# Performance work log

Measured on AMD Instinct MI355X. Metric: run time of the kernel, lower is better.

The kernel has to match this reference:

```python
import jax, jax.numpy as jnp
import numpy as np

E, T, D, N_RBF, N_SBF = 262144, 1048576, 128, 6, 42


def setup_inputs() -> dict:
    key = jax.random.key(0)
    ks = jax.random.split(key, 24)
    s = 0.05
    inp = {
        "m_ji": jax.random.normal(ks[0], (E, D), jnp.float32),
        "e_rbf": jax.random.normal(ks[1], (E, N_RBF), jnp.float32),
        "a_sbf": jax.random.normal(ks[2], (T, N_SBF), jnp.float32),
        "nbr_list": jax.random.randint(ks[3], (E, 2), 0, 65536),
        "kj_idx": jax.random.randint(ks[4], (T,), 0, E),
        "ji_idx": jax.random.randint(ks[5], (T,), 0, E),
        # edge branch params
        "We": jax.random.normal(ks[6], (N_RBF, D), jnp.float32) * s,
        "W_e1": jax.random.normal(ks[7], (D, D), jnp.float32) * s,
        "b_e1": jnp.zeros((D,), jnp.float32),
        "W_e2": jax.random.normal(ks[8], (D, D), jnp.float32) * s,
        "b_e2": jnp.zeros((D,), jnp.float32),
        "W_e3": jax.random.normal(ks[9], (D, D), jnp.float32) * s,
        "b_e3": jnp.zeros((D,), jnp.float32),
        "W_e4": jax.random.normal(ks[10], (D, D), jnp.float32) * s,
        # angle branch params
        "Wa": jax.random.normal(ks[11], (N_SBF, D), jnp.float32) * s,
        "W_a1": jax.random.normal(ks[12], (D, D), jnp.float32) * s,
        "b_a1": jnp.zeros((D,), jnp.float32),
        "W_a2": jax.random.normal(ks[13], (D, D), jnp.float32) * s,
        "b_a2": jnp.zeros((D,), jnp.float32),
        "W_a3": jax.random.normal(ks[14], (D, D), jnp.float32) * s,
        "b_a3": jnp.zeros((D,), jnp.float32),
        "W_a4": jax.random.normal(ks[15], (D, D), jnp.float32) * s,
    }
    return inp


def _mlp(x, W1, b1, W2, b2, W3, b3, W4):
    x = jax.nn.silu(x @ W1 + b1)
    x = jax.nn.silu(x @ W2 + b2)
    x = jax.nn.silu(x @ W3 + b3)
    return x @ W4


def reference(m_ji, e_rbf, a_sbf, nbr_list, kj_idx, ji_idx,
              We, W_e1, b_e1, W_e2, b_e2, W_e3, b_e3, W_e4,
              Wa, W_a1, b_a1, W_a2, b_a2, W_a3, b_a3, W_a4):
    # edge branch: project rbf to embed dim, gate by edge messages  [E, D]
    edge_feats = _mlp((e_rbf @ We) * m_ji, W_e1, b_e1, W_e2, b_e2, W_e3, b_e3, W_e4)
    # angle branch: project sbf, gate by triplet-gathered message sum  [T, D]
    angle_gate = m_ji[kj_idx] + m_ji[ji_idx]
    angle_feats = _mlp((a_sbf @ Wa) * angle_gate, W_a1, b_a1, W_a2, b_a2, W_a3, b_a3, W_a4)
    return (edge_feats, angle_feats)
```

## Files before the change

kernel.cpp:

```cpp
#include <hip/hip_runtime.h>
#include <stdint.h>

typedef __attribute__((ext_vector_type(8))) short bf16x8;
typedef __attribute__((ext_vector_type(4))) float f32x4;
typedef __attribute__((ext_vector_type(8))) unsigned short us8;

#define T_CNT 1048576
#define E_CNT 262144

static __device__ __forceinline__ unsigned short f2bf_u(float f) {
  __bf16 h = (__bf16)f;
  return __builtin_bit_cast(unsigned short, h);
}
static __device__ __forceinline__ uint32_t pack2bf(float a, float b) {
  return (uint32_t)f2bf_u(a) | ((uint32_t)f2bf_u(b) << 16);
}
static __device__ __forceinline__ float silu_f(float v) {
  float e = __builtin_amdgcn_exp2f(v * -1.44269504088896341f);
  return v * __builtin_amdgcn_rcpf(1.0f + e);
}
static __device__ __forceinline__ bf16x8 frag8(f32x4 a, f32x4 b) {
  bf16x8 r;
  r[0] = (short)f2bf_u(a[0]); r[1] = (short)f2bf_u(a[1]);
  r[2] = (short)f2bf_u(a[2]); r[3] = (short)f2bf_u(a[3]);
  r[4] = (short)f2bf_u(b[0]); r[5] = (short)f2bf_u(b[1]);
  r[6] = (short)f2bf_u(b[2]); r[7] = (short)f2bf_u(b[3]);
  return r;
}

__global__ __launch_bounds__(256)
__attribute__((amdgpu_waves_per_eu(4, 5)))
void angle_kernel(
    const float* __restrict__ m_ji, const float* __restrict__ a_sbf,
    const int* __restrict__ kj, const int* __restrict__ ji,
    const float* __restrict__ b1, const float* __restrict__ b2,
    const float* __restrict__ b3,
    const char* __restrict__ wt4, const char* __restrict__ waT,
    float* __restrict__ out)
{
  __shared__ __align__(16) char xbA[16384];
  __shared__ __align__(16) char xbB[16384];
  const int tid = threadIdx.x, lane = tid & 63, w = tid >> 6;
  const int l15 = lane & 15, q = lane >> 4;
  const int rs = (l15 & 7) << 4;
  const size_t tb = (size_t)blockIdx.x * 64;
  const int cb = w * 32;

  bf16x8 wa[2][2];
  #pragma unroll
  for (int ct = 0; ct < 2; ++ct)
    #pragma unroll
    for (int ks = 0; ks < 2; ++ks)
      wa[ct][ks] = *(const bf16x8*)(waT + (((w * 2 + ct) * 2 + ks) << 10) + lane * 16);

  int ikj[4], iji[4];
  #pragma unroll
  for (int g = 0; g < 4; ++g) {
    ikj[g] = kj[tb + g * 16 + l15];
    iji[g] = ji[tb + g * 16 + l15];
  }

  f32x4 pk[2][2], pj[2][2];
  auto gissue = [&](int g) {
    const float* bk = m_ji + (size_t)ikj[g] * 128 + cb + q * 4;
    const float* bj = m_ji + (size_t)iji[g] * 128 + cb + q * 4;
    pk[g & 1][0] = *(const f32x4*)(bk);
    pk[g & 1][1] = *(const f32x4*)(bk + 16);
    pj[g & 1][0] = *(const f32x4*)(bj);
    pj[g & 1][1] = *(const f32x4*)(bj + 16);
  };
  gissue(0); gissue(1);

  #pragma unroll
  for (int rg = 0; rg < 4; ++rg) {
    const int row = rg * 16 + l15;
    const float* ap = a_sbf + (tb + row) * 42;
    f32x4 a0 = *(const f32x4*)(ap + q * 8);
    f32x4 a1 = *(const f32x4*)(ap + q * 8 + 4);
    f32x4 c0 = {0.f, 0.f, 0.f, 0.f}, c1 = {0.f, 0.f, 0.f, 0.f};
    if (q == 0) { c0 = *(const f32x4*)(ap + 32); c1 = *(const f32x4*)(ap + 36); }
    else if (q == 1) { float2 t = *(const float2*)(ap + 40); c0[0] = t.x; c0[1] = t.y; }
    bf16x8 f0 = frag8(a0, a1);
    bf16x8 f1 = frag8(c0, c1);
    f32x4 acc0 = {0.f, 0.f, 0.f, 0.f}, acc1 = {0.f, 0.f, 0.f, 0.f};
    acc0 = __builtin_amdgcn_mfma_f32_16x16x32_bf16(wa[0][0], f0, acc0, 0, 0, 0);
    acc0 = __builtin_amdgcn_mfma_f32_16x16x32_bf16(wa[0][1], f1, acc0, 0, 0, 0);
    acc1 = __builtin_amdgcn_mfma_f32_16x16x32_bf16(wa[1][0], f0, acc1, 0, 0, 0);
    acc1 = __builtin_amdgcn_mfma_f32_16x16x32_bf16(wa[1][1], f1, acc1, 0, 0, 0);
    f32x4 g0 = pk[rg & 1][0] + pj[rg & 1][0];
    f32x4 g1 = pk[rg & 1][1] + pj[rg & 1][1];
    if (rg < 2) gissue(rg + 2);
    uint2 u0, u1;
    u0.x = pack2bf(acc0[0] * g0[0], acc0[1] * g0[1]);
    u0.y = pack2bf(acc0[2] * g0[2], acc0[3] * g0[3]);
    u1.x = pack2bf(acc1[0] * g1[0], acc1[1] * g1[1]);
    u1.y = pack2bf(acc1[2] * g1[2], acc1[3] * g1[3]);
    *(uint2*)(xbA + ((row * 256 + w * 64 + q * 8) ^ rs)) = u0;
    *(uint2*)(xbA + ((row * 256 + w * 64 + 32 + q * 8) ^ rs)) = u1;
  }
  __syncthreads();

  #pragma unroll
  for (int L = 0; L < 4; ++L) {
    const char* src = (L & 1) ? xbB : xbA;
    char* dst = (L & 1) ? xbA : xbB;
    bf16x8 wf[2][4];
    #pragma unroll
    for (int ct = 0; ct < 2; ++ct)
      #pragma unroll
      for (int ks = 0; ks < 4; ++ks)
        wf[ct][ks] = *(const bf16x8*)(wt4 + (L << 15) + (((w * 2 + ct) * 4 + ks) << 10) + lane * 16);
    if (L < 3) {
      const float* bp = (L == 0) ? b1 : (L == 1) ? b2 : b3;
      f32x4 bv0 = *(const f32x4*)(bp + cb + q * 4);
      f32x4 bv1 = *(const f32x4*)(bp + cb + 16 + q * 4);
      #pragma unroll
      for (int rg = 0; rg < 4; ++rg) {
        const int row = rg * 16 + l15;
        f32x4 acc0 = {0.f, 0.f, 0.f, 0.f}, acc1 = {0.f, 0.f, 0.f, 0.f};
        #pragma unroll
        for (int ks = 0; ks < 4; ++ks) {
          bf16x8 xf = *(const bf16x8*)(src + ((row * 256 + ks * 64 + q * 16) ^ rs));
          acc0 = __builtin_amdgcn_mfma_f32_16x16x32_bf16(wf[0][ks], xf, acc0, 0, 0, 0);
          acc1 = __builtin_amdgcn_mfma_f32_16x16x32_bf16(wf[1][ks], xf, acc1, 0, 0, 0);
        }
        uint2 u0, u1;
        u0.x = pack2bf(silu_f(acc0[0] + bv0[0]), silu_f(acc0[1] + bv0[1]));
        u0.y = pack2bf(silu_f(acc0[2] + bv0[2]), silu_f(acc0[3] + bv0[3]));
        u1.x = pack2bf(silu_f(acc1[0] + bv1[0]), silu_f(acc1[1] + bv1[1]));
        u1.y = pack2bf(silu_f(acc1[2] + bv1[2]), silu_f(acc1[3] + bv1[3]));
        *(uint2*)(dst + ((row * 256 + w * 64 + q * 8) ^ rs)) = u0;
        *(uint2*)(dst + ((row * 256 + w * 64 + 32 + q * 8) ^ rs)) = u1;
      }
      __syncthreads();
    } else {
      #pragma unroll
      for (int rg = 0; rg < 4; ++rg) {
        const int row = rg * 16 + l15;
        f32x4 acc0 = {0.f, 0.f, 0.f, 0.f}, acc1 = {0.f, 0.f, 0.f, 0.f};
        #pragma unroll
        for (int ks = 0; ks < 4; ++ks) {
          bf16x8 xf = *(const bf16x8*)(src + ((row * 256 + ks * 64 + q * 16) ^ rs));
          acc0 = __builtin_amdgcn_mfma_f32_16x16x32_bf16(wf[0][ks], xf, acc0, 0, 0, 0);
          acc1 = __builtin_amdgcn_mfma_f32_16x16x32_bf16(wf[1][ks], xf, acc1, 0, 0, 0);
        }
        float* op = out + (tb + row) * 128 + cb + q * 4;
        __builtin_nontemporal_store(acc0, (f32x4*)(op));
        __builtin_nontemporal_store(acc1, (f32x4*)(op + 16));
      }
    }
  }
}

__global__ __launch_bounds__(256)
__attribute__((amdgpu_waves_per_eu(4, 5)))
void edge_kernel(
    const float* __restrict__ m_ji, const float* __restrict__ e_rbf,
    const float* __restrict__ b1, const float* __restrict__ b2,
    const float* __restrict__ b3,
    const char* __restrict__ wt4, const char* __restrict__ weT,
    float* __restrict__ out)
{
  __shared__ __align__(16) char xbA[16384];
  __shared__ __align__(16) char xbB[16384];
  const int tid = threadIdx.x, lane = tid & 63, w = tid >> 6;
  const int l15 = lane & 15, q = lane >> 4;
  const int rs = (l15 & 7) << 4;
  const size_t tb = (size_t)blockIdx.x * 64;
  const int cb = w * 32;

  bf16x8 we[2];
  #pragma unroll
  for (int ct = 0; ct < 2; ++ct)
    we[ct] = *(const bf16x8*)(weT + ((w * 2 + ct) << 10) + lane * 16);

  f32x4 mr[2][2];
  auto missue = [&](int g) {
    const float* bm = m_ji + (tb + g * 16 + l15) * 128 + cb + q * 4;
    mr[g & 1][0] = *(const f32x4*)(bm);
    mr[g & 1][1] = *(const f32x4*)(bm + 16);
  };
  missue(0); missue(1);

  #pragma unroll
  for (int rg = 0; rg < 4; ++rg) {
    const int row = rg * 16 + l15;
    const float* ep = e_rbf + (tb + row) * 6;
    f32x4 a0 = {0.f, 0.f, 0.f, 0.f}, a1 = {0.f, 0.f, 0.f, 0.f};
    if (q == 0) {
      a0 = *(const f32x4*)(ep);
      float2 t = *(const float2*)(ep + 4);
      a1[0] = t.x; a1[1] = t.y;
    }
    bf16x8 ef = frag8(a0, a1);
    f32x4 acc0 = {0.f, 0.f, 0.f, 0.f}, acc1 = {0.f, 0.f, 0.f, 0.f};
    acc0 = __builtin_amdgcn_mfma_f32_16x16x32_bf16(we[0], ef, acc0, 0, 0, 0);
    acc1 = __builtin_amdgcn_mfma_f32_16x16x32_bf16(we[1], ef, acc1, 0, 0, 0);
    f32x4 g0 = mr[rg & 1][0];
    f32x4 g1 = mr[rg & 1][1];
    if (rg < 2) missue(rg + 2);
    uint2 u0, u1;
    u0.x = pack2bf(acc0[0] * g0[0], acc0[1] * g0[1]);
    u0.y = pack2bf(acc0[2] * g0[2], acc0[3] * g0[3]);
    u1.x = pack2bf(acc1[0] * g1[0], acc1[1] * g1[1]);
    u1.y = pack2bf(acc1[2] * g1[2], acc1[3] * g1[3]);
    *(uint2*)(xbA + ((row * 256 + w * 64 + q * 8) ^ rs)) = u0;
    *(uint2*)(xbA + ((row * 256 + w * 64 + 32 + q * 8) ^ rs)) = u1;
  }
  __syncthreads();

  #pragma unroll
  for (int L = 0; L < 4; ++L) {
    const char* src = (L & 1) ? xbB : xbA;
    char* dst = (L & 1) ? xbA : xbB;
    bf16x8 wf[2][4];
    #pragma unroll
    for (int ct = 0; ct < 2; ++ct)
      #pragma unroll
      for (int ks = 0; ks < 4; ++ks)
        wf[ct][ks] = *(const bf16x8*)(wt4 + (L << 15) + (((w * 2 + ct) * 4 + ks) << 10) + lane * 16);
    if (L < 3) {
      const float* bp = (L == 0) ? b1 : (L == 1) ? b2 : b3;
      f32x4 bv0 = *(const f32x4*)(bp + cb + q * 4);
      f32x4 bv1 = *(const f32x4*)(bp + cb + 16 + q * 4);
      #pragma unroll
      for (int rg = 0; rg < 4; ++rg) {
        const int row = rg * 16 + l15;
        f32x4 acc0 = {0.f, 0.f, 0.f, 0.f}, acc1 = {0.f, 0.f, 0.f, 0.f};
        #pragma unroll
        for (int ks = 0; ks < 4; ++ks) {
          bf16x8 xf = *(const bf16x8*)(src + ((row * 256 + ks * 64 + q * 16) ^ rs));
          acc0 = __builtin_amdgcn_mfma_f32_16x16x32_bf16(wf[0][ks], xf, acc0, 0, 0, 0);
          acc1 = __builtin_amdgcn_mfma_f32_16x16x32_bf16(wf[1][ks], xf, acc1, 0, 0, 0);
        }
        uint2 u0, u1;
        u0.x = pack2bf(silu_f(acc0[0] + bv0[0]), silu_f(acc0[1] + bv0[1]));
        u0.y = pack2bf(silu_f(acc0[2] + bv0[2]), silu_f(acc0[3] + bv0[3]));
        u1.x = pack2bf(silu_f(acc1[0] + bv1[0]), silu_f(acc1[1] + bv1[1]));
        u1.y = pack2bf(silu_f(acc1[2] + bv1[2]), silu_f(acc1[3] + bv1[3]));
        *(uint2*)(dst + ((row * 256 + w * 64 + q * 8) ^ rs)) = u0;
        *(uint2*)(dst + ((row * 256 + w * 64 + 32 + q * 8) ^ rs)) = u1;
      }
      __syncthreads();
    } else {
      #pragma unroll
      for (int rg = 0; rg < 4; ++rg) {
        const int row = rg * 16 + l15;
        f32x4 acc0 = {0.f, 0.f, 0.f, 0.f}, acc1 = {0.f, 0.f, 0.f, 0.f};
        #pragma unroll
        for (int ks = 0; ks < 4; ++ks) {
          bf16x8 xf = *(const bf16x8*)(src + ((row * 256 + ks * 64 + q * 16) ^ rs));
          acc0 = __builtin_amdgcn_mfma_f32_16x16x32_bf16(wf[0][ks], xf, acc0, 0, 0, 0);
          acc1 = __builtin_amdgcn_mfma_f32_16x16x32_bf16(wf[1][ks], xf, acc1, 0, 0, 0);
        }
        float* op = out + (tb + row) * 128 + cb + q * 4;
        __builtin_nontemporal_store(acc0, (f32x4*)(op));
        __builtin_nontemporal_store(acc1, (f32x4*)(op + 16));
      }
    }
  }
}

__global__ void prep_kernel(
    const float* __restrict__ W0, const float* __restrict__ W1,
    const float* __restrict__ W2, const float* __restrict__ W3,
    const float* __restrict__ W4, const float* __restrict__ W5,
    const float* __restrict__ W6, const float* __restrict__ W7,
    const float* __restrict__ Wa, const float* __restrict__ We,
    char* __restrict__ ws)
{
  const int gid = blockIdx.x * 256 + threadIdx.x;
  const int lane = gid & 63;
  const int l15 = lane & 15, q = lane >> 4;
  if (gid < 16384) {
    const int mat = gid >> 11;
    const int ctks = (gid & 2047) >> 6;
    const int n = (ctks >> 2) * 16 + l15;
    const int k0 = (ctks & 3) * 32 + q * 8;
    const float* W;
    switch (mat) {
      case 0: W = W0; break; case 1: W = W1; break;
      case 2: W = W2; break; case 3: W = W3; break;
      case 4: W = W4; break; case 5: W = W5; break;
      case 6: W = W6; break; default: W = W7; break;
    }
    us8 v;
    #pragma unroll
    for (int j = 0; j < 8; ++j) v[j] = f2bf_u(W[(size_t)(k0 + j) * 128 + n]);
    *(us8*)(ws + mat * 32768 + ctks * 1024 + lane * 16) = v;
  } else if (gid < 17408) {
    const int g = gid - 16384;
    const int ctks = g >> 6;
    const int n = (ctks >> 1) * 16 + l15;
    const int k0 = (ctks & 1) * 32 + q * 8;
    us8 v;
    #pragma unroll
    for (int j = 0; j < 8; ++j) {
      const int k = k0 + j;
      v[j] = (k < 42) ? f2bf_u(Wa[(size_t)k * 128 + n]) : (unsigned short)0;
    }
    *(us8*)(ws + 262144 + ctks * 1024 + lane * 16) = v;
  } else if (gid < 17920) {
    const int g = gid - 17408;
    const int ct = g >> 6;
    const int n = ct * 16 + l15;
    const int k0 = q * 8;
    us8 v;
    #pragma unroll
    for (int j = 0; j < 8; ++j) {
      const int k = k0 + j;
      v[j] = (k < 6) ? f2bf_u(We[(size_t)k * 128 + n]) : (unsigned short)0;
    }
    *(us8*)(ws + 278528 + ct * 1024 + lane * 16) = v;
  }
}

extern "C" void kernel_launch(void* const* d_in, const int* in_sizes, int n_in,
                              void* d_out, int out_size, void* d_ws, size_t ws_size,
                              hipStream_t stream) {
  (void)in_sizes; (void)n_in; (void)out_size; (void)ws_size;
  const float* m_ji  = (const float*)d_in[0];
  const float* e_rbf = (const float*)d_in[1];
  const float* a_sbf = (const float*)d_in[2];
  const int*   kj    = (const int*)d_in[4];
  const int*   ji    = (const int*)d_in[5];
  const float* We    = (const float*)d_in[6];
  const float* We1   = (const float*)d_in[7];
  const float* be1   = (const float*)d_in[8];
  const float* We2   = (const float*)d_in[9];
  const float* be2   = (const float*)d_in[10];
  const float* We3   = (const float*)d_in[11];
  const float* be3   = (const float*)d_in[12];
  const float* We4   = (const float*)d_in[13];
  const float* Wa    = (const float*)d_in[14];
  const float* Wa1   = (const float*)d_in[15];
  const float* ba1   = (const float*)d_in[16];
  const float* Wa2   = (const float*)d_in[17];
  const float* ba2   = (const float*)d_in[18];
  const float* Wa3   = (const float*)d_in[19];
  const float* ba3   = (const float*)d_in[20];
  const float* Wa4   = (const float*)d_in[21];
  char* ws = (char*)d_ws;
  float* out = (float*)d_out;

  prep_kernel<<<70, 256, 0, stream>>>(
      We1, We2, We3, We4, Wa1, Wa2, Wa3, Wa4, Wa, We, ws);
  edge_kernel<<<E_CNT / 64, 256, 0, stream>>>(
      m_ji, e_rbf, be1, be2, be3, ws, ws + 278528, out);
  angle_kernel<<<T_CNT / 64, 256, 0, stream>>>(
      m_ji, a_sbf, kj, ji, ba1, ba2, ba3, ws + 131072, ws + 262144,
      out + (size_t)E_CNT * 128);
}
```

Baseline: 525.6 us.

## Split angle branch into gather/projection kernel and MLP kernel via workspace

Splits the angle branch in two when the workspace is large enough. The first kernel does the gather of m_ji rows, the sbf projection and the gating, and writes a bf16 activation buffer to the workspace. The second kernel streams that buffer into LDS with global_load_lds and runs the 4-layer MLP. The goal is to keep the latency-bound random gathers out of the MFMA-heavy kernel and let each kernel use the occupancy that suits it. The cost is an extra round trip of about 256 MB of intermediate data through global memory, and the waves_per_eu hints are dropped.

```diff
diff --git a/kernel.cpp b/kernel.cpp
--- a/kernel.cpp
+++ b/kernel.cpp
@@ -4,6 +4,8 @@
 typedef __attribute__((ext_vector_type(8))) short bf16x8;
 typedef __attribute__((ext_vector_type(4))) float f32x4;
 typedef __attribute__((ext_vector_type(8))) unsigned short us8;
+typedef __attribute__((ext_vector_type(2))) unsigned int u32x2;
+typedef __bf16 bf16v2 __attribute__((ext_vector_type(2)));
 
 #define T_CNT 1048576
 #define E_CNT 262144
@@ -13,93 +15,33 @@
   return __builtin_bit_cast(unsigned short, h);
 }
 static __device__ __forceinline__ uint32_t pack2bf(float a, float b) {
-  return (uint32_t)f2bf_u(a) | ((uint32_t)f2bf_u(b) << 16);
+  bf16v2 t; t[0] = (__bf16)a; t[1] = (__bf16)b;
+  return __builtin_bit_cast(uint32_t, t);
 }
 static __device__ __forceinline__ float silu_f(float v) {
   float e = __builtin_amdgcn_exp2f(v * -1.44269504088896341f);
   return v * __builtin_amdgcn_rcpf(1.0f + e);
 }
 static __device__ __forceinline__ bf16x8 frag8(f32x4 a, f32x4 b) {
-  bf16x8 r;
-  r[0] = (short)f2bf_u(a[0]); r[1] = (short)f2bf_u(a[1]);
-  r[2] = (short)f2bf_u(a[2]); r[3] = (short)f2bf_u(a[3]);
-  r[4] = (short)f2bf_u(b[0]); r[5] = (short)f2bf_u(b[1]);
-  r[6] = (short)f2bf_u(b[2]); r[7] = (short)f2bf_u(b[3]);
-  return r;
-}
-
-__global__ __launch_bounds__(256)
-__attribute__((amdgpu_waves_per_eu(4, 5)))
-void angle_kernel(
-    const float* __restrict__ m_ji, const float* __restrict__ a_sbf,
-    const int* __restrict__ kj, const int* __restrict__ ji,
+  union { bf16x8 v; uint32_t u[4]; } r;
+  r.u[0] = pack2bf(a[0], a[1]); r.u[1] = pack2bf(a[2], a[3]);
+  r.u[2] = pack2bf(b[0], b[1]); r.u[3] = pack2bf(b[2], b[3]);
+  return r.v;
+}
+static __device__ __forceinline__ void gl_lds16(const void* g, void* l) {
+  __builtin_amdgcn_global_load_lds(
+      (const __attribute__((address_space(1))) void*)g,
+      (__attribute__((address_space(3))) void*)l, 16, 0, 0);
+}
+
+static __device__ __forceinline__ void mlp4(
+    char* __restrict__ xbA, char* __restrict__ xbB,
+    const char* __restrict__ wt4,
     const float* __restrict__ b1, const float* __restrict__ b2,
-    const float* __restrict__ b3,
-    const char* __restrict__ wt4, const char* __restrict__ waT,
-    float* __restrict__ out)
-{
-  __shared__ __align__(16) char xbA[16384];
-  __shared__ __align__(16) char xbB[16384];
-  const int tid = threadIdx.x, lane = tid & 63, w = tid >> 6;
-  const int l15 = lane & 15, q = lane >> 4;
-  const int rs = (l15 & 7) << 4;
-  const size_t tb = (size_t)blockIdx.x * 64;
+    const float* __restrict__ b3, float* __restrict__ outT,
+    int l15, int q, int w, int rs)
+{
   const int cb = w * 32;
-
-  bf16x8 wa[2][2];
-  #pragma unroll
-  for (int ct = 0; ct < 2; ++ct)
-    #pragma unroll
-    for (int ks = 0; ks < 2; ++ks)
-      wa[ct][ks] = *(const bf16x8*)(waT + (((w * 2 + ct) * 2 + ks) << 10) + lane * 16);
-
-  int ikj[4], iji[4];
-  #pragma unroll
-  for (int g = 0; g < 4; ++g) {
-    ikj[g] = kj[tb + g * 16 + l15];
-    iji[g] = ji[tb + g * 16 + l15];
-  }
-
-  f32x4 pk[2][2], pj[2][2];
-  auto gissue = [&](int g) {
-    const float* bk = m_ji + (size_t)ikj[g] * 128 + cb + q * 4;
-    const float* bj = m_ji + (size_t)iji[g] * 128 + cb + q * 4;
-    pk[g & 1][0] = *(const f32x4*)(bk);
-    pk[g & 1][1] = *(const f32x4*)(bk + 16);
-    pj[g & 1][0] = *(const f32x4*)(bj);
-    pj[g & 1][1] = *(const f32x4*)(bj + 16);
-  };
-  gissue(0); gissue(1);
-
-  #pragma unroll
-  for (int rg = 0; rg < 4; ++rg) {
-    const int row = rg * 16 + l15;
-    const float* ap = a_sbf + (tb + row) * 42;
-    f32x4 a0 = *(const f32x4*)(ap + q * 8);
-    f32x4 a1 = *(const f32x4*)(ap + q * 8 + 4);
-    f32x4 c0 = {0.f, 0.f, 0.f, 0.f}, c1 = {0.f, 0.f, 0.f, 0.f};
-    if (q == 0) { c0 = *(const f32x4*)(ap + 32); c1 = *(const f32x4*)(ap + 36); }
-    else if (q == 1) { float2 t = *(const float2*)(ap + 40); c0[0] = t.x; c0[1] = t.y; }
-    bf16x8 f0 = frag8(a0, a1);
-    bf16x8 f1 = frag8(c0, c1);
-    f32x4 acc0 = {0.f, 0.f, 0.f, 0.f}, acc1 = {0.f, 0.f, 0.f, 0.f};
-    acc0 = __builtin_amdgcn_mfma_f32_16x16x32_bf16(wa[0][0], f0, acc0, 0, 0, 0);
-    acc0 = __builtin_amdgcn_mfma_f32_16x16x32_bf16(wa[0][1], f1, acc0, 0, 0, 0);
-    acc1 = __builtin_amdgcn_mfma_f32_16x16x32_bf16(wa[1][0], f0, acc1, 0, 0, 0);
-    acc1 = __builtin_amdgcn_mfma_f32_16x16x32_bf16(wa[1][1], f1, acc1, 0, 0, 0);
-    f32x4 g0 = pk[rg & 1][0] + pj[rg & 1][0];
-    f32x4 g1 = pk[rg & 1][1] + pj[rg & 1][1];
-    if (rg < 2) gissue(rg + 2);
-    uint2 u0, u1;
-    u0.x = pack2bf(acc0[0] * g0[0], acc0[1] * g0[1]);
-    u0.y = pack2bf(acc0[2] * g0[2], acc0[3] * g0[3]);
-    u1.x = pack2bf(acc1[0] * g1[0], acc1[1] * g1[1]);
-    u1.y = pack2bf(acc1[2] * g1[2], acc1[3] * g1[3]);
-    *(uint2*)(xbA + ((row * 256 + w * 64 + q * 8) ^ rs)) = u0;
-    *(uint2*)(xbA + ((row * 256 + w * 64 + 32 + q * 8) ^ rs)) = u1;
-  }
-  __syncthreads();
-
   #pragma unroll
   for (int L = 0; L < 4; ++L) {
     const char* src = (L & 1) ? xbB : xbA;
@@ -109,7 +51,7 @@
     for (int ct = 0; ct < 2; ++ct)
       #pragma unroll
       for (int ks = 0; ks < 4; ++ks)
-        wf[ct][ks] = *(const bf16x8*)(wt4 + (L << 15) + (((w * 2 + ct) * 4 + ks) << 10) + lane * 16);
+        wf[ct][ks] = *(const bf16x8*)(wt4 + (L << 15) + (((w * 2 + ct) * 4 + ks) << 10) + (l15 | (q << 4)) * 16);
     if (L < 3) {
       const float* bp = (L == 0) ? b1 : (L == 1) ? b2 : b3;
       f32x4 bv0 = *(const f32x4*)(bp + cb + q * 4);
@@ -117,7 +59,7 @@
       #pragma unroll
       for (int rg = 0; rg < 4; ++rg) {
         const int row = rg * 16 + l15;
-        f32x4 acc0 = {0.f, 0.f, 0.f, 0.f}, acc1 = {0.f, 0.f, 0.f, 0.f};
+        f32x4 acc0 = {0.f,0.f,0.f,0.f}, acc1 = {0.f,0.f,0.f,0.f};
         #pragma unroll
         for (int ks = 0; ks < 4; ++ks) {
           bf16x8 xf = *(const bf16x8*)(src + ((row * 256 + ks * 64 + q * 16) ^ rs));
@@ -137,14 +79,14 @@
       #pragma unroll
       for (int rg = 0; rg < 4; ++rg) {
         const int row = rg * 16 + l15;
-        f32x4 acc0 = {0.f, 0.f, 0.f, 0.f}, acc1 = {0.f, 0.f, 0.f, 0.f};
+        f32x4 acc0 = {0.f,0.f,0.f,0.f}, acc1 = {0.f,0.f,0.f,0.f};
         #pragma unroll
         for (int ks = 0; ks < 4; ++ks) {
           bf16x8 xf = *(const bf16x8*)(src + ((row * 256 + ks * 64 + q * 16) ^ rs));
           acc0 = __builtin_amdgcn_mfma_f32_16x16x32_bf16(wf[0][ks], xf, acc0, 0, 0, 0);
           acc1 = __builtin_amdgcn_mfma_f32_16x16x32_bf16(wf[1][ks], xf, acc1, 0, 0, 0);
         }
-        float* op = out + (tb + row) * 128 + cb + q * 4;
+        float* op = outT + (size_t)row * 128 + cb + q * 4;
         __builtin_nontemporal_store(acc0, (f32x4*)(op));
         __builtin_nontemporal_store(acc1, (f32x4*)(op + 16));
       }
@@ -152,13 +94,85 @@
   }
 }
 
-__global__ __launch_bounds__(256)
-__attribute__((amdgpu_waves_per_eu(4, 5)))
-void edge_kernel(
-    const float* __restrict__ m_ji, const float* __restrict__ e_rbf,
+__global__ __launch_bounds__(256) void angle_proj_kernel(
+    const float* __restrict__ m_ji, const float* __restrict__ a_sbf,
+    const int* __restrict__ kj, const int* __restrict__ ji,
+    const char* __restrict__ waT, char* __restrict__ x0)
+{
+  const int tid = threadIdx.x, lane = tid & 63, w = tid >> 6;
+  const int l15 = lane & 15, q = lane >> 4;
+  const int rs = (l15 & 7) << 4;
+  const size_t tb = (size_t)blockIdx.x * 64;
+  const int rl = w * 16 + l15;
+  const size_t grow = tb + rl;
+
+  const int ikj = kj[grow], iji = ji[grow];
+  const float* bk = m_ji + (size_t)ikj * 128 + q * 4;
+  const float* bj = m_ji + (size_t)iji * 128 + q * 4;
+
+  f32x4 pk[4], pj[4];
+  #pragma unroll
+  for (int g = 0; g < 4; ++g) {
+    pk[g] = *(const f32x4*)(bk + g * 16);
+    pj[g] = *(const f32x4*)(bj + g * 16);
+  }
+
+  const float* ap = a_sbf + grow * 42;
+  f32x4 a0 = *(const f32x4*)(ap + q * 8);
+  f32x4 a1 = *(const f32x4*)(ap + q * 8 + 4);
+  f32x4 c0 = {0.f,0.f,0.f,0.f}, c1 = {0.f,0.f,0.f,0.f};
+  if (q == 0) { c0 = *(const f32x4*)(ap + 32); c1 = *(const f32x4*)(ap + 36); }
+  else if (q == 1) { float2 t = *(const float2*)(ap + 40); c0[0] = t.x; c0[1] = t.y; }
+  bf16x8 f0 = frag8(a0, a1);
+  bf16x8 f1 = frag8(c0, c1);
+
+  char* xrow = x0 + tb * 256 + rl * 256;
+  #pragma unroll
+  for (int c = 0; c < 8; ++c) {
+    bf16x8 wa0 = *(const bf16x8*)(waT + ((c * 2 + 0) << 10) + lane * 16);
+    bf16x8 wa1 = *(const bf16x8*)(waT + ((c * 2 + 1) << 10) + lane * 16);
+    f32x4 acc = {0.f,0.f,0.f,0.f};
+    acc = __builtin_amdgcn_mfma_f32_16x16x32_bf16(wa0, f0, acc, 0, 0, 0);
+    acc = __builtin_amdgcn_mfma_f32_16x16x32_bf16(wa1, f1, acc, 0, 0, 0);
+    f32x4 g = pk[c & 3] + pj[c & 3];
+    if (c < 4) {
+      pk[c & 3] = *(const f32x4*)(bk + (c + 4) * 16);
+      pj[c & 3] = *(const f32x4*)(bj + (c + 4) * 16);
+    }
+    u32x2 u;
+    u[0] = pack2bf(acc[0] * g[0], acc[1] * g[1]);
+    u[1] = pack2bf(acc[2] * g[2], acc[3] * g[3]);
+    __builtin_nontemporal_store(u, (u32x2*)(xrow + ((c * 32 + q * 8) ^ rs)));
+  }
+}
+
+__global__ __launch_bounds__(256) void angle_mlp_kernel(
+    const char* __restrict__ x0,
     const float* __restrict__ b1, const float* __restrict__ b2,
     const float* __restrict__ b3,
-    const char* __restrict__ wt4, const char* __restrict__ weT,
+    const char* __restrict__ wt4, float* __restrict__ out)
+{
+  __shared__ __align__(16) char xbA[16384];
+  __shared__ __align__(16) char xbB[16384];
+  const int tid = threadIdx.x, lane = tid & 63, w = tid >> 6;
+  const int l15 = lane & 15, q = lane >> 4;
+  const int rs = (l15 & 7) << 4;
+  const size_t tb = (size_t)blockIdx.x * 64;
+
+  #pragma unroll
+  for (int i = 0; i < 4; ++i)
+    gl_lds16(x0 + tb * 256 + i * 4096 + tid * 16, xbA + i * 4096 + tid * 16);
+  __syncthreads();
+
+  mlp4(xbA, xbB, wt4, b1, b2, b3, out + tb * 128, l15, q, w, rs);
+}
+
+__global__ __launch_bounds__(256) void angle_fused_kernel(
+    const float* __restrict__ m_ji, const float* __restrict__ a_sbf,
+    const int* __restrict__ kj, const int* __restrict__ ji,
+    const float* __restrict__ b1, const float* __restrict__ b2,
+    const float* __restrict__ b3,
+    const char* __restrict__ wt4, const char* __restrict__ waT,
     float* __restrict__ out)
 {
   __shared__ __align__(16) char xbA[16384];
@@ -169,6 +183,77 @@
   const size_t tb = (size_t)blockIdx.x * 64;
   const int cb = w * 32;
 
+  bf16x8 wa[2][2];
+  #pragma unroll
+  for (int ct = 0; ct < 2; ++ct)
+    #pragma unroll
+    for (int ks = 0; ks < 2; ++ks)
+      wa[ct][ks] = *(const bf16x8*)(waT + (((w * 2 + ct) * 2 + ks) << 10) + lane * 16);
+
+  int ikj[4], iji[4];
+  #pragma unroll
+  for (int g = 0; g < 4; ++g) {
+    ikj[g] = kj[tb + g * 16 + l15];
+    iji[g] = ji[tb + g * 16 + l15];
+  }
+  f32x4 pk[2][2], pj[2][2];
+  auto gissue = [&](int g) {
+    const float* bk = m_ji + (size_t)ikj[g] * 128 + cb + q * 4;
+    const float* bj = m_ji + (size_t)iji[g] * 128 + cb + q * 4;
+    pk[g & 1][0] = *(const f32x4*)(bk);
+    pk[g & 1][1] = *(const f32x4*)(bk + 16);
+    pj[g & 1][0] = *(const f32x4*)(bj);
+    pj[g & 1][1] = *(const f32x4*)(bj + 16);
+  };
+  gissue(0); gissue(1);
+
+  #pragma unroll
+  for (int rg = 0; rg < 4; ++rg) {
+    const int row = rg * 16 + l15;
+    const float* ap = a_sbf + (tb + row) * 42;
+    f32x4 a0 = *(const f32x4*)(ap + q * 8);
+    f32x4 a1 = *(const f32x4*)(ap + q * 8 + 4);
+    f32x4 c0 = {0.f,0.f,0.f,0.f}, c1 = {0.f,0.f,0.f,0.f};
+    if (q == 0) { c0 = *(const f32x4*)(ap + 32); c1 = *(const f32x4*)(ap + 36); }
+    else if (q == 1) { float2 t = *(const float2*)(ap + 40); c0[0] = t.x; c0[1] = t.y; }
+    bf16x8 f0 = frag8(a0, a1);
+    bf16x8 f1 = frag8(c0, c1);
+    f32x4 acc0 = {0.f,0.f,0.f,0.f}, acc1 = {0.f,0.f,0.f,0.f};
+    acc0 = __builtin_amdgcn_mfma_f32_16x16x32_bf16(wa[0][0], f0, acc0, 0, 0, 0);
+    acc0 = __builtin_amdgcn_mfma_f32_16x16x32_bf16(wa[0][1], f1, acc0, 0, 0, 0);
+    acc1 = __builtin_amdgcn_mfma_f32_16x16x32_bf16(wa[1][0], f0, acc1, 0, 0, 0);
+    acc1 = __builtin_amdgcn_mfma_f32_16x16x32_bf16(wa[1][1], f1, acc1, 0, 0, 0);
+    f32x4 g0 = pk[rg & 1][0] + pj[rg & 1][0];
+    f32x4 g1 = pk[rg & 1][1] + pj[rg & 1][1];
+    if (rg < 2) gissue(rg + 2);
+    uint2 u0, u1;
+    u0.x = pack2bf(acc0[0] * g0[0], acc0[1] * g0[1]);
+    u0.y = pack2bf(acc0[2] * g0[2], acc0[3] * g0[3]);
+    u1.x = pack2bf(acc1[0] * g1[0], acc1[1] * g1[1]);
+    u1.y = pack2bf(acc1[2] * g1[2], acc1[3] * g1[3]);
+    *(uint2*)(xbA + ((row * 256 + w * 64 + q * 8) ^ rs)) = u0;
+    *(uint2*)(xbA + ((row * 256 + w * 64 + 32 + q * 8) ^ rs)) = u1;
+  }
+  __syncthreads();
+
+  mlp4(xbA, xbB, wt4, b1, b2, b3, out + tb * 128, l15, q, w, rs);
+}
+
+__global__ __launch_bounds__(256) void edge_kernel(
+    const float* __restrict__ m_ji, const float* __restrict__ e_rbf,
+    const float* __restrict__ b1, const float* __restrict__ b2,
+    const float* __restrict__ b3,
+    const char* __restrict__ wt4, const char* __restrict__ weT,
+    float* __restrict__ out)
+{
+  __shared__ __align__(16) char xbA[16384];
+  __shared__ __align__(16) char xbB[16384];
+  const int tid = threadIdx.x, lane = tid & 63, w = tid >> 6;
+  const int l15 = lane & 15, q = lane >> 4;
+  const int rs = (l15 & 7) << 4;
+  const size_t tb = (size_t)blockIdx.x * 64;
+  const int cb = w * 32;
+
   bf16x8 we[2];
   #pragma unroll
   for (int ct = 0; ct < 2; ++ct)
@@ -186,14 +271,14 @@
   for (int rg = 0; rg < 4; ++rg) {
     const int row = rg * 16 + l15;
     const float* ep = e_rbf + (tb + row) * 6;
-    f32x4 a0 = {0.f, 0.f, 0.f, 0.f}, a1 = {0.f, 0.f, 0.f, 0.f};
+    f32x4 a0 = {0.f,0.f,0.f,0.f}, a1 = {0.f,0.f,0.f,0.f};
     if (q == 0) {
       a0 = *(const f32x4*)(ep);
       float2 t = *(const float2*)(ep + 4);
       a1[0] = t.x; a1[1] = t.y;
     }
     bf16x8 ef = frag8(a0, a1);
-    f32x4 acc0 = {0.f, 0.f, 0.f, 0.f}, acc1 = {0.f, 0.f, 0.f, 0.f};
+    f32x4 acc0 = {0.f,0.f,0.f,0.f}, acc1 = {0.f,0.f,0.f,0.f};
     acc0 = __builtin_amdgcn_mfma_f32_16x16x32_bf16(we[0], ef, acc0, 0, 0, 0);
     acc1 = __builtin_amdgcn_mfma_f32_16x16x32_bf16(we[1], ef, acc1, 0, 0, 0);
     f32x4 g0 = mr[rg & 1][0];
@@ -209,56 +294,7 @@
   }
   __syncthreads();
 
-  #pragma unroll
-  for (int L = 0; L < 4; ++L) {
-    const char* src = (L & 1) ? xbB : xbA;
-    char* dst = (L & 1) ? xbA : xbB;
-    bf16x8 wf[2][4];
-    #pragma unroll
-    for (int ct = 0; ct < 2; ++ct)
-      #pragma unroll
-      for (int ks = 0; ks < 4; ++ks)
-        wf[ct][ks] = *(const bf16x8*)(wt4 + (L << 15) + (((w * 2 + ct) * 4 + ks) << 10) + lane * 16);
-    if (L < 3) {
-      const float* bp = (L == 0) ? b1 : (L == 1) ? b2 : b3;
-      f32x4 bv0 = *(const f32x4*)(bp + cb + q * 4);
-      f32x4 bv1 = *(const f32x4*)(bp + cb + 16 + q * 4);
-      #pragma unroll
-      for (int rg = 0; rg < 4; ++rg) {
-        const int row = rg * 16 + l15;
-        f32x4 acc0 = {0.f, 0.f, 0.f, 0.f}, acc1 = {0.f, 0.f, 0.f, 0.f};
-        #pragma unroll
-        for (int ks = 0; ks < 4; ++ks) {
-          bf16x8 xf = *(const bf16x8*)(src + ((row * 256 + ks * 64 + q * 16) ^ rs));
-          acc0 = __builtin_amdgcn_mfma_f32_16x16x32_bf16(wf[0][ks], xf, acc0, 0, 0, 0);
-          acc1 = __builtin_amdgcn_mfma_f32_16x16x32_bf16(wf[1][ks], xf, acc1, 0, 0, 0);
-        }
-        uint2 u0, u1;
-        u0.x = pack2bf(silu_f(acc0[0] + bv0[0]), silu_f(acc0[1] + bv0[1]));
-        u0.y = pack2bf(silu_f(acc0[2] + bv0[2]), silu_f(acc0[3] + bv0[3]));
-        u1.x = pack2bf(silu_f(acc1[0] + bv1[0]), silu_f(acc1[1] + bv1[1]));
-        u1.y = pack2bf(silu_f(acc1[2] + bv1[2]), silu_f(acc1[3] + bv1[3]));
-        *(uint2*)(dst + ((row * 256 + w * 64 + q * 8) ^ rs)) = u0;
-        *(uint2*)(dst + ((row * 256 + w * 64 + 32 + q * 8) ^ rs)) = u1;
-      }
-      __syncthreads();
-    } else {
-      #pragma unroll
-      for (int rg = 0; rg < 4; ++rg) {
-        const int row = rg * 16 + l15;
-        f32x4 acc0 = {0.f, 0.f, 0.f, 0.f}, acc1 = {0.f, 0.f, 0.f, 0.f};
-        #pragma unroll
-        for (int ks = 0; ks < 4; ++ks) {
-          bf16x8 xf = *(const bf16x8*)(src + ((row * 256 + ks * 64 + q * 16) ^ rs));
-          acc0 = __builtin_amdgcn_mfma_f32_16x16x32_bf16(wf[0][ks], xf, acc0, 0, 0, 0);
-          acc1 = __builtin_amdgcn_mfma_f32_16x16x32_bf16(wf[1][ks], xf, acc1, 0, 0, 0);
-        }
-        float* op = out + (tb + row) * 128 + cb + q * 4;
-        __builtin_nontemporal_store(acc0, (f32x4*)(op));
-        __builtin_nontemporal_store(acc1, (f32x4*)(op + 16));
-      }
-    }
-  }
+  mlp4(xbA, xbB, wt4, b1, b2, b3, out + tb * 128, l15, q, w, rs);
 }
 
 __global__ void prep_kernel(
@@ -318,7 +354,7 @@
 extern "C" void kernel_launch(void* const* d_in, const int* in_sizes, int n_in,
                               void* d_out, int out_size, void* d_ws, size_t ws_size,
                               hipStream_t stream) {
-  (void)in_sizes; (void)n_in; (void)out_size; (void)ws_size;
+  (void)in_sizes; (void)n_in; (void)out_size;
   const float* m_ji  = (const float*)d_in[0];
   const float* e_rbf = (const float*)d_in[1];
   const float* a_sbf = (const float*)d_in[2];
@@ -342,12 +378,23 @@
   const float* Wa4   = (const float*)d_in[21];
   char* ws = (char*)d_ws;
   float* out = (float*)d_out;
+  float* out_a = out + (size_t)E_CNT * 128;
 
   prep_kernel<<<70, 256, 0, stream>>>(
       We1, We2, We3, We4, Wa1, Wa2, Wa3, Wa4, Wa, We, ws);
   edge_kernel<<<E_CNT / 64, 256, 0, stream>>>(
       m_ji, e_rbf, be1, be2, be3, ws, ws + 278528, out);
-  angle_kernel<<<T_CNT / 64, 256, 0, stream>>>(
-      m_ji, a_sbf, kj, ji, ba1, ba2, ba3, ws + 131072, ws + 262144,
-      out + (size_t)E_CNT * 128);
-}
+
+  const size_t x0_off = 1u << 20;
+  const size_t need = x0_off + (size_t)T_CNT * 256;
+  if (ws_size >= need) {
+    char* x0 = ws + x0_off;
+    angle_proj_kernel<<<T_CNT / 64, 256, 0, stream>>>(
+        m_ji, a_sbf, kj, ji, ws + 262144, x0);
+    angle_mlp_kernel<<<T_CNT / 64, 256, 0, stream>>>(
+        x0, ba1, ba2, ba3, ws + 131072, out_a);
+  } else {
+    angle_fused_kernel<<<T_CNT / 64, 256, 0, stream>>>(
+        m_ji, a_sbf, kj, ji, ba1, ba2, ba3, ws + 131072, ws + 262144, out_a);
+  }
+}
```

Measured after the change: 596.2 us. 13.4% more time.
